# Kernel optimization log

Hardware: AMD Instinct MI355X
Metric: run time of the kernel (lower is better)

Reference implementation:

```python
import jax, jax.numpy as jnp
import numpy as np

B, IN, OUT = 16384, 4096, 4096


def setup_inputs() -> dict:
    key = jax.random.key(0)
    k1, k2, k3 = jax.random.split(key, 3)
    x = jax.random.normal(k1, (B, IN), dtype=jnp.float32)
    full_precision = jax.random.normal(k2, (OUT, IN), dtype=jnp.float32) * 0.02
    bias = jax.random.normal(k3, (OUT,), dtype=jnp.float32) * 0.02
    return {"x": x, "full_precision": full_precision, "bias": bias}


def reference(x, full_precision, bias):
    # In-place param preprocessing from the torch module:
    # center each weight row, then clamp to [-1, 1].
    fp = full_precision - jnp.mean(full_precision, axis=1, keepdims=True)
    fp = jnp.clip(fp, -1.0, 1.0)
    # BinActive: sign of the activations (dropout_ratio == 0, so no dropout).
    xb = jnp.sign(x)
    # Binary weight: sign(fp) scaled by per-output-row mean absolute value.
    mean_val = jnp.mean(jnp.abs(fp), axis=1, keepdims=True)  # [OUT, 1]
    w = jnp.sign(fp) * mean_val                               # [OUT, IN]
    # Dense linear: [B, IN] @ [IN, OUT] + [OUT]
    return xb @ w.T + bias
```

## Files before the change

### kernel.cpp

```cpp
#include <hip/hip_runtime.h>
#include <cstdint>

#define B_SZ   16384
#define IN_SZ  4096
#define OUT_SZ 4096

typedef int int4v  __attribute__((ext_vector_type(4)));
typedef int int16v __attribute__((ext_vector_type(16)));

__device__ __forceinline__ int sgn8(float v) { return (v > 0.f) - (v < 0.f); }

__global__ __launch_bounds__(256) void wprep_kernel(const float* __restrict__ fp,
                                                    int8_t* __restrict__ wb,
                                                    float* __restrict__ alpha) {
    __shared__ float red[4];
    const int o = blockIdx.x;
    const int t = threadIdx.x;
    const float4* row = (const float4*)(fp + (size_t)o * IN_SZ);

    float4 v[4];
    float s = 0.f;
#pragma unroll
    for (int i = 0; i < 4; ++i) {
        v[i] = row[t + i * 256];
        s += (v[i].x + v[i].y) + (v[i].z + v[i].w);
    }
#pragma unroll
    for (int off = 32; off > 0; off >>= 1) s += __shfl_down(s, off, 64);
    if ((t & 63) == 0) red[t >> 6] = s;
    __syncthreads();
    const float mean = (red[0] + red[1] + red[2] + red[3]) * (1.f / IN_SZ);
    __syncthreads();

    int* wrow = (int*)(wb + (size_t)o * IN_SZ);
    float a = 0.f;
#pragma unroll
    for (int i = 0; i < 4; ++i) {
        const float dx = v[i].x - mean, dy = v[i].y - mean;
        const float dz = v[i].z - mean, dw = v[i].w - mean;
        a += fminf(fabsf(dx), 1.f) + fminf(fabsf(dy), 1.f)
           + fminf(fabsf(dz), 1.f) + fminf(fabsf(dw), 1.f);
        const int p = (sgn8(dx) & 0xff) | ((sgn8(dy) & 0xff) << 8)
                    | ((sgn8(dz) & 0xff) << 16) | (sgn8(dw) << 24);
        wrow[t + i * 256] = p;
    }
#pragma unroll
    for (int off = 32; off > 0; off >>= 1) a += __shfl_down(a, off, 64);
    if ((t & 63) == 0) red[t >> 6] = a;
    __syncthreads();
    if (t == 0) alpha[o] = (red[0] + red[1] + red[2] + red[3]) * (1.f / IN_SZ);
}

__global__ __launch_bounds__(256) void xprep_kernel(const float* __restrict__ x,
                                                    int8_t* __restrict__ xb) {
    const size_t i = ((size_t)blockIdx.x * 256 + threadIdx.x) * 2;
    const float4 v0 = ((const float4*)x)[i];
    const float4 v1 = ((const float4*)x)[i + 1];
    int2 p;
    p.x = (sgn8(v0.x) & 0xff) | ((sgn8(v0.y) & 0xff) << 8)
        | ((sgn8(v0.z) & 0xff) << 16) | (sgn8(v0.w) << 24);
    p.y = (sgn8(v1.x) & 0xff) | ((sgn8(v1.y) & 0xff) << 8)
        | ((sgn8(v1.z) & 0xff) << 16) | (sgn8(v1.w) << 24);
    ((int2*)xb)[i / 2] = p;
}

__global__ __launch_bounds__(256, 4) void gemm_kernel(const int8_t* __restrict__ Xb,
                                                      const int8_t* __restrict__ Wb,
                                                      const float* __restrict__ alpha,
                                                      const float* __restrict__ bias,
                                                      float* __restrict__ out) {
    __shared__ __align__(16) int8_t As[128 * 64];
    __shared__ __align__(16) int8_t Bs[128 * 64];

    const int tid  = threadIdx.x;
    const int lane = tid & 63;
    const int wave = tid >> 6;
    const int tm = blockIdx.x;
    const int tn = blockIdx.y;
    const int wm = (wave >> 1) * 64;
    const int wn = (wave & 1) * 64;

    const int srow = lane >> 2;
    const int scol = (lane & 3) * 16;
    const int8_t* gA = Xb + (size_t)(tm * 128 + wave * 32 + srow) * IN_SZ + scol;
    const int8_t* gB = Wb + (size_t)(tn * 128 + wave * 32 + srow) * IN_SZ + scol;

    int16v acc[2][2] = {};

    const int frow = lane & 31;
    const int fk   = (lane >> 5) * 16;

    for (int k0 = 0; k0 < IN_SZ; k0 += 64) {
#pragma unroll
        for (int j = 0; j < 2; ++j) {
            __builtin_amdgcn_global_load_lds(
                (const __attribute__((address_space(1))) uint32_t*)(gA + k0 + (size_t)j * 16 * IN_SZ),
                (__attribute__((address_space(3))) uint32_t*)(As + (wave * 32 + j * 16) * 64),
                16, 0, 0);
            __builtin_amdgcn_global_load_lds(
                (const __attribute__((address_space(1))) uint32_t*)(gB + k0 + (size_t)j * 16 * IN_SZ),
                (__attribute__((address_space(3))) uint32_t*)(Bs + (wave * 32 + j * 16) * 64),
                16, 0, 0);
        }
        __syncthreads();

#pragma unroll
        for (int s = 0; s < 2; ++s) {
            int4v a[2], b[2];
#pragma unroll
            for (int i = 0; i < 2; ++i) {
                a[i] = *(const int4v*)(As + (wm + i * 32 + frow) * 64 + s * 32 + fk);
                b[i] = *(const int4v*)(Bs + (wn + i * 32 + frow) * 64 + s * 32 + fk);
            }
#pragma unroll
            for (int i = 0; i < 2; ++i)
#pragma unroll
                for (int j = 0; j < 2; ++j)
                    acc[i][j] = __builtin_amdgcn_mfma_i32_32x32x32_i8(a[i], b[j], acc[i][j], 0, 0, 0);
        }
        __syncthreads();
    }

    const int col = lane & 31;
    const int rbase = 4 * (lane >> 5);
#pragma unroll
    for (int j = 0; j < 2; ++j) {
        const int o = tn * 128 + wn + j * 32 + col;
        const float al = alpha[o];
        const float bi = bias[o];
#pragma unroll
        for (int i = 0; i < 2; ++i) {
            const size_t mbase = (size_t)(tm * 128 + wm + i * 32);
#pragma unroll
            for (int r = 0; r < 16; ++r) {
                const int row = (r & 3) + 8 * (r >> 2) + rbase;
                out[(mbase + row) * OUT_SZ + o] = al * (float)acc[i][j][r] + bi;
            }
        }
    }
}

extern "C" void kernel_launch(void* const* d_in, const int* in_sizes, int n_in,
                              void* d_out, int out_size, void* d_ws, size_t ws_size,
                              hipStream_t stream) {
    const float* x    = (const float*)d_in[0];
    const float* fp   = (const float*)d_in[1];
    const float* bias = (const float*)d_in[2];
    float* out = (float*)d_out;

    int8_t* xb    = (int8_t*)d_ws;
    int8_t* wb    = xb + (size_t)B_SZ * IN_SZ;
    float*  alpha = (float*)(wb + (size_t)OUT_SZ * IN_SZ);

    hipLaunchKernelGGL(wprep_kernel, dim3(OUT_SZ), dim3(256), 0, stream, fp, wb, alpha);
    hipLaunchKernelGGL(xprep_kernel, dim3(B_SZ * IN_SZ / 2048), dim3(256), 0, stream, x, xb);
    hipLaunchKernelGGL(gemm_kernel, dim3(B_SZ / 128, OUT_SZ / 128), dim3(256), 0, stream,
                       xb, wb, alpha, bias, out);
}
```

Measured before the change: 814.6 us.

## Enlarge GEMM tile, double-buffer LDS, swizzle, remap blocks, nontemporal stores

The int8 GEMM tile grows from 128x128 to 256x128, so each wave holds 4x2 MFMA accumulators and data reuse per LDS load rises. The LDS tiles are double-buffered so the next K slice loads while the current one is computed, which also removes one barrier wait per iteration. LDS columns are XOR-swizzled to avoid bank conflicts, and a 1D grid is remapped (XCD interleave plus grouped M tiles) to improve L2 locality. Output is written with nontemporal stores. Occupancy drops to 3 blocks per CU because of the extra registers and LDS.

```diff
diff --git a/kernel.cpp b/kernel.cpp
--- a/kernel.cpp
+++ b/kernel.cpp
@@ -64,61 +64,79 @@
     ((int2*)xb)[i / 2] = p;
 }
 
-__global__ __launch_bounds__(256, 4) void gemm_kernel(const int8_t* __restrict__ Xb,
+__global__ __launch_bounds__(256, 3) void gemm_kernel(const int8_t* __restrict__ Xb,
                                                       const int8_t* __restrict__ Wb,
                                                       const float* __restrict__ alpha,
                                                       const float* __restrict__ bias,
                                                       float* __restrict__ out) {
-    __shared__ __align__(16) int8_t As[128 * 64];
-    __shared__ __align__(16) int8_t Bs[128 * 64];
+    __shared__ __align__(16) int8_t As[2][256 * 64];
+    __shared__ __align__(16) int8_t Bs[2][128 * 64];
 
     const int tid  = threadIdx.x;
     const int lane = tid & 63;
     const int wave = tid >> 6;
-    const int tm = blockIdx.x;
-    const int tn = blockIdx.y;
-    const int wm = (wave >> 1) * 64;
+
+    const int bid     = blockIdx.x;
+    const int logical = (bid & 7) * 256 + (bid >> 3);
+    const int group   = logical >> 7;
+    const int rem     = logical & 127;
+    const int tm = group * 4 + (rem & 3);
+    const int tn = rem >> 2;
+
+    const int wm = (wave >> 1) * 128;
     const int wn = (wave & 1) * 64;
 
     const int srow = lane >> 2;
-    const int scol = (lane & 3) * 16;
-    const int8_t* gA = Xb + (size_t)(tm * 128 + wave * 32 + srow) * IN_SZ + scol;
+    const int scol = ((lane & 3) ^ ((lane >> 3) & 3)) << 4;
+    const int8_t* gA = Xb + (size_t)(tm * 256 + wave * 64 + srow) * IN_SZ + scol;
     const int8_t* gB = Wb + (size_t)(tn * 128 + wave * 32 + srow) * IN_SZ + scol;
 
-    int16v acc[2][2] = {};
+    int16v acc[4][2] = {};
 
-    const int frow = lane & 31;
-    const int fk   = (lane >> 5) * 16;
+    const int frow  = lane & 31;
+    const int khalf = lane >> 5;
+    const int fxor  = (lane >> 1) & 3;
 
-    for (int k0 = 0; k0 < IN_SZ; k0 += 64) {
+    auto stage = [&](int bb, int k0) {
 #pragma unroll
-        for (int j = 0; j < 2; ++j) {
+        for (int j = 0; j < 4; ++j)
             __builtin_amdgcn_global_load_lds(
                 (const __attribute__((address_space(1))) uint32_t*)(gA + k0 + (size_t)j * 16 * IN_SZ),
-                (__attribute__((address_space(3))) uint32_t*)(As + (wave * 32 + j * 16) * 64),
+                (__attribute__((address_space(3))) uint32_t*)(&As[bb][(wave * 64 + j * 16) * 64]),
                 16, 0, 0);
+#pragma unroll
+        for (int j = 0; j < 2; ++j)
             __builtin_amdgcn_global_load_lds(
                 (const __attribute__((address_space(1))) uint32_t*)(gB + k0 + (size_t)j * 16 * IN_SZ),
-                (__attribute__((address_space(3))) uint32_t*)(Bs + (wave * 32 + j * 16) * 64),
+                (__attribute__((address_space(3))) uint32_t*)(&Bs[bb][(wave * 32 + j * 16) * 64]),
                 16, 0, 0);
-        }
-        __syncthreads();
+    };
+
+    stage(0, 0);
+    __syncthreads();
+
+    int bb = 0;
+    for (int k0 = 0; k0 < IN_SZ; k0 += 64) {
+        if (k0 + 64 < IN_SZ) stage(bb ^ 1, k0 + 64);
 
 #pragma unroll
         for (int s = 0; s < 2; ++s) {
-            int4v a[2], b[2];
+            const int chunk = ((s * 2 + khalf) ^ fxor) << 4;
+            int4v a[4], b[2];
 #pragma unroll
-            for (int i = 0; i < 2; ++i) {
-                a[i] = *(const int4v*)(As + (wm + i * 32 + frow) * 64 + s * 32 + fk);
-                b[i] = *(const int4v*)(Bs + (wn + i * 32 + frow) * 64 + s * 32 + fk);
-            }
+            for (int i = 0; i < 4; ++i)
+                a[i] = *(const int4v*)(&As[bb][(wm + i * 32 + frow) * 64 + chunk]);
 #pragma unroll
-            for (int i = 0; i < 2; ++i)
+            for (int j = 0; j < 2; ++j)
+                b[j] = *(const int4v*)(&Bs[bb][(wn + j * 32 + frow) * 64 + chunk]);
+#pragma unroll
+            for (int i = 0; i < 4; ++i)
 #pragma unroll
                 for (int j = 0; j < 2; ++j)
                     acc[i][j] = __builtin_amdgcn_mfma_i32_32x32x32_i8(a[i], b[j], acc[i][j], 0, 0, 0);
         }
         __syncthreads();
+        bb ^= 1;
     }
 
     const int col = lane & 31;
@@ -129,12 +147,13 @@
         const float al = alpha[o];
         const float bi = bias[o];
 #pragma unroll
-        for (int i = 0; i < 2; ++i) {
-            const size_t mbase = (size_t)(tm * 128 + wm + i * 32);
+        for (int i = 0; i < 4; ++i) {
+            const size_t mbase = (size_t)(tm * 256 + wm + i * 32);
 #pragma unroll
             for (int r = 0; r < 16; ++r) {
                 const int row = (r & 3) + 8 * (r >> 2) + rbase;
-                out[(mbase + row) * OUT_SZ + o] = al * (float)acc[i][j][r] + bi;
+                __builtin_nontemporal_store(al * (float)acc[i][j][r] + bi,
+                                            &out[(mbase + row) * OUT_SZ + o]);
             }
         }
     }
@@ -154,6 +173,6 @@
 
     hipLaunchKernelGGL(wprep_kernel, dim3(OUT_SZ), dim3(256), 0, stream, fp, wb, alpha);
     hipLaunchKernelGGL(xprep_kernel, dim3(B_SZ * IN_SZ / 2048), dim3(256), 0, stream, x, xb);
-    hipLaunchKernelGGL(gemm_kernel, dim3(B_SZ / 128, OUT_SZ / 128), dim3(256), 0, stream,
+    hipLaunchKernelGGL(gemm_kernel, dim3((B_SZ / 256) * (OUT_SZ / 128)), dim3(256), 0, stream,
                        xb, wb, alpha, bias, out);
 }
```

Result: faster. 756.1 us (-7.2%).
